# Performance work log

Measured on AMD Instinct MI355X. Metric: run time of the kernel, lower is better.

Reference implementation:

```python
import jax, jax.numpy as jnp
import numpy as np

N_NODES = 20000
N_EDGES = 320000
NUM_FEATURES = 128
HIDDEN = 128
NUM_CLASSES = 40
GRID_SIZE = 4
SPLINE_ORDER = 3
NB = GRID_SIZE + SPLINE_ORDER  # basis functions per input feature
_H = 2.0 / GRID_SIZE  # grid_range [-1, 1]
GRID = jnp.arange(-SPLINE_ORDER, GRID_SIZE + SPLINE_ORDER + 1, dtype=jnp.float32) * _H - 1.0


def b_splines(x):
    # x: (N, in) -> (N, in, NB) via Cox-de Boor recursion (efficient-KAN)
    xg = x[..., None]
    b = ((xg >= GRID[:-1]) & (xg < GRID[1:])).astype(x.dtype)
    for k in range(1, SPLINE_ORDER + 1):
        b = ((xg - GRID[: -(k + 1)]) / (GRID[k:-1] - GRID[: -(k + 1)]) * b[..., :-1]
             + (GRID[k + 1:] - xg) / (GRID[k + 1:] - GRID[1:-k]) * b[..., 1:])
    return b


def kan_linear(x, base_w, spline_w):
    # base branch: silu(x) @ W_base^T ; spline branch: contraction over (in, NB)
    base = jax.nn.silu(x) @ base_w.T
    spline = jnp.einsum('nik,oik->no', b_splines(x), spline_w)
    return base + spline


def gcn_conv(h, base_w, spline_w, bias, src_f, dst_f, norm):
    h = kan_linear(h, base_w, spline_w)
    msg = h[src_f] * norm[:, None]  # gather + edge scaling
    out = jax.ops.segment_sum(msg, dst_f, num_segments=N_NODES)
    return out + bias


def batchnorm(h, gamma, beta):
    mean = h.mean(axis=0)
    var = h.var(axis=0)  # biased, as torch BN uses for normalization
    return (h - mean) * jax.lax.rsqrt(var + 1e-5) * gamma + beta


def setup_inputs() -> dict:
    key = jax.random.key(0)
    ks = jax.random.split(key, 8)
    s = 0.1
    return {
        'x': jax.random.normal(ks[0], (N_NODES, NUM_FEATURES), dtype=jnp.float32),
        'edge_index': jax.random.randint(ks[1], (2, N_EDGES), 0, N_NODES, dtype=jnp.int64),
        'base_w0': jax.random.normal(ks[2], (HIDDEN, NUM_FEATURES), dtype=jnp.float32) * s,
        'spline_w0': jax.random.normal(ks[3], (HIDDEN, NUM_FEATURES, NB), dtype=jnp.float32) * s,
        'bias0': jnp.zeros((HIDDEN,), dtype=jnp.float32),
        'base_w1': jax.random.normal(ks[4], (HIDDEN, HIDDEN), dtype=jnp.float32) * s,
        'spline_w1': jax.random.normal(ks[5], (HIDDEN, HIDDEN, NB), dtype=jnp.float32) * s,
        'bias1': jnp.zeros((HIDDEN,), dtype=jnp.float32),
        'base_w_out': jax.random.normal(ks[6], (NUM_CLASSES, NUM_FEATURES + 2 * HIDDEN), dtype=jnp.float32) * s,
        'spline_w_out': jax.random.normal(ks[7], (NUM_CLASSES, NUM_FEATURES + 2 * HIDDEN, NB), dtype=jnp.float32) * s,
        'bias_out': jnp.zeros((NUM_CLASSES,), dtype=jnp.float32),
        'gamma': jnp.ones((HIDDEN,), dtype=jnp.float32),
        'beta': jnp.zeros((HIDDEN,), dtype=jnp.float32),
    }


def reference(x, edge_index, base_w0, spline_w0, bias0, base_w1, spline_w1, bias1,
              base_w_out, spline_w_out, bias_out, gamma, beta):
    # gcn_norm with self loops (computed once, reused by every layer)
    loop = jnp.arange(N_NODES, dtype=edge_index.dtype)
    src_f = jnp.concatenate([edge_index[0], loop])
    dst_f = jnp.concatenate([edge_index[1], loop])
    deg = jax.ops.segment_sum(jnp.ones_like(dst_f, dtype=x.dtype), dst_f, num_segments=N_NODES)
    dinv = jnp.where(deg > 0, jax.lax.rsqrt(jnp.maximum(deg, 1e-12)), 0.0)
    norm = dinv[src_f] * dinv[dst_f]

    skips = [x]
    h = x
    for bw, sw, b in ((base_w0, spline_w0, bias0), (base_w1, spline_w1, bias1)):
        h = gcn_conv(h, bw, sw, b, src_f, dst_f, norm)
        h = batchnorm(h, gamma, beta)  # shared BN, dropout p=0.0 is identity
        skips.append(h)
    h = jnp.concatenate(skips, axis=1)  # (N, 128 + 2*128)
    return gcn_conv(h, base_w_out, spline_w_out, bias_out, src_f, dst_f, norm)
```

## Files before the change

### kernel.cpp

```cpp
#include <hip/hip_runtime.h>

#define NN 20000
#define NPAD 20064

typedef _Float16 half8 __attribute__((ext_vector_type(8)));
typedef _Float16 half2v __attribute__((ext_vector_type(2)));
typedef float floatx4 __attribute__((ext_vector_type(4)));

#define MFMA16(a, b, c) __builtin_amdgcn_mfma_f32_16x16x32_f16((a), (b), (c), 0, 0, 0)
#define LD8(p) (*(const half8*)(p))
#define SBAR() __builtin_amdgcn_sched_barrier(0)

__device__ __forceinline__ void bspline7(float x, float b[7]) {
  float t[10];
#pragma unroll
  for (int i = 0; i < 10; ++i) {
    float g = -2.5f + 0.5f * (float)i;
    t[i] = (x >= g && x < g + 0.5f) ? 1.0f : 0.0f;
  }
#pragma unroll
  for (int i = 0; i < 9; ++i) {
    float g = -2.5f + 0.5f * (float)i;
    t[i] = ((x - g) * t[i] + (g + 1.0f - x) * t[i + 1]) * 2.0f;
  }
#pragma unroll
  for (int i = 0; i < 8; ++i) {
    float g = -2.5f + 0.5f * (float)i;
    t[i] = ((x - g) * t[i] + (g + 1.5f - x) * t[i + 1]);
  }
#pragma unroll
  for (int i = 0; i < 7; ++i) {
    float g = -2.5f + 0.5f * (float)i;
    b[i] = ((x - g) * t[i] + (g + 2.0f - x) * t[i + 1]) * (1.0f / 1.5f);
  }
}

__device__ __forceinline__ float silu_f(float x) {
  return x * (1.0f / (1.0f + __expf(-x)));
}

__device__ __forceinline__ void build_lds(const float* __restrict__ X,
                                          const float* __restrict__ ss, int has_bn,
                                          int row0, int tid, _Float16* __restrict__ Fs) {
  for (int idx = tid; idx < 32 * 128; idx += 256) {
    int r = idx >> 7, i = idx & 127;
    int row = row0 + r;
    float xv = (row < NN) ? X[(size_t)row * 128 + i] : 0.0f;
    if (has_bn) xv = xv * ss[i] + ss[128 + i];
    float b[7];
    bspline7(xv, b);
    half8 hv;
    hv[0] = (_Float16)silu_f(xv);
#pragma unroll
    for (int k = 0; k < 7; ++k) hv[k + 1] = (_Float16)b[k];
    *(half8*)(Fs + ((size_t)r * 128 + (i ^ (r & 7))) * 8) = hv;
  }
}

__global__ void packw_all(const float* __restrict__ Wb0, const float* __restrict__ Ws0,
                          const float* __restrict__ Wb1, const float* __restrict__ Ws1,
                          const float* __restrict__ WbO, const float* __restrict__ WsO,
                          _Float16* __restrict__ WPA0, _Float16* __restrict__ WPA1,
                          _Float16* __restrict__ WPC) {
  int bid = blockIdx.x;
  if (bid < 1536) {
    int s = (bid >= 768) ? 1 : 0;
    int idx = (bid - s * 768) * 256 + threadIdx.x;
    if (idx >= 196608) return;
    const float* Wb = s ? Wb1 : Wb0;
    const float* Wsp = s ? Ws1 : Ws0;
    _Float16* WP = s ? WPA1 : WPA0;
    int jj = idx & 7;
    int lane = (idx >> 3) & 63;
    int u = idx >> 9;
    int cb = u % 12, ks = u / 12;
    int i = ks * 4 + (lane >> 4);
    int orow = lane & 15;
    float v = 0.0f;
    if (cb < 8) {
      int o = cb * 16 + orow;
      v = (jj == 0) ? Wb[(size_t)o * 128 + i] : Wsp[(size_t)o * 896 + i * 7 + (jj - 1)];
    } else {
      int o = (cb - 8) * 16 + orow;
      if (o < 40)
        v = (jj == 0) ? WbO[(size_t)o * 384 + s * 128 + i]
                      : WsO[(size_t)o * 2688 + s * 896 + i * 7 + (jj - 1)];
    }
    WP[idx] = (_Float16)v;
  } else {
    int idx = (bid - 1536) * 256 + threadIdx.x;
    if (idx >= 65536) return;
    int jj = idx & 7;
    int lane = (idx >> 3) & 63;
    int u = idx >> 9;
    int cb = u & 3, ks = u >> 2;
    int i = ks * 4 + (lane >> 4);
    int o = cb * 16 + (lane & 15);
    float v = 0.0f;
    if (o < 40)
      v = (jj == 0) ? WbO[(size_t)o * 384 + 2 * 128 + i]
                    : WsO[(size_t)o * 2688 + 2 * 896 + i * 7 + (jj - 1)];
    WPC[idx] = (_Float16)v;
  }
}

__global__ void count_deg(const int* __restrict__ dst, int* __restrict__ degE, int E) {
  int e = blockIdx.x * 256 + threadIdx.x;
  if (e < E) atomicAdd(&degE[dst[e]], 1);
}

__global__ void build_meta2(const int* __restrict__ degE, int* __restrict__ rowptr,
                            int* __restrict__ cursor, float* __restrict__ dinv, int n) {
  __shared__ int wsum[16];
  int tid = threadIdx.x, lane = tid & 63, wid = tid >> 6;
  int i0 = tid * 20;
  int d[20];
  int s = 0;
#pragma unroll
  for (int j = 0; j < 20; ++j) {
    int i = i0 + j;
    int v = (i < n) ? degE[i] : 0;
    d[j] = v;
    s += v;
    if (i < n) dinv[i] = rsqrtf((float)(v + 1));
  }
  int val = s;
#pragma unroll
  for (int off = 1; off < 64; off <<= 1) {
    int t = __shfl_up(val, off);
    if (lane >= off) val += t;
  }
  if (lane == 63) wsum[wid] = val;
  __syncthreads();
  if (wid == 0) {
    int wv = (lane < 16) ? wsum[lane] : 0;
#pragma unroll
    for (int off = 1; off < 16; off <<= 1) {
      int t = __shfl_up(wv, off);
      if (lane >= off) wv += t;
    }
    if (lane < 16) wsum[lane] = wv;
  }
  __syncthreads();
  int base = (wid ? wsum[wid - 1] : 0) + val - s;
  if (tid == 0) rowptr[0] = 0;
#pragma unroll
  for (int j = 0; j < 20; ++j) {
    int i = i0 + j;
    if (i < n) {
      cursor[i] = base;
      rowptr[i + 1] = base + d[j];
      base += d[j];
    }
  }
}

__global__ void fill_csr(const int* __restrict__ src, const int* __restrict__ dst,
                         int* __restrict__ cursor, int* __restrict__ csr, int E) {
  int e = blockIdx.x * 256 + threadIdx.x;
  if (e < E) {
    int p = atomicAdd(&cursor[dst[e]], 1);
    csr[p] = src[e];
  }
}

__global__ __launch_bounds__(256) void gemmFA(const float* __restrict__ X,
                                              const float* __restrict__ ss, int has_bn,
                                              const _Float16* __restrict__ WP,
                                              const float* __restrict__ dinv,
                                              _Float16* __restrict__ A, float* __restrict__ P) {
  __shared__ _Float16 Fs[32 * 1024];
  int tid = threadIdx.x;
  int lane = tid & 63, cg = tid >> 6;
  int row0 = blockIdx.x * 32;
  build_lds(X, ss, has_bn, row0, tid, Fs);
  __syncthreads();
  int rx = lane & 7, kg = lane >> 4;
  const _Float16* Fr0 = Fs + (size_t)(lane & 15) * 1024;
  const _Float16* Fr1 = Fr0 + 16 * 1024;
  const _Float16* Bp = WP + ((size_t)(cg * 3) * 64 + lane) * 8;
  floatx4 acc0 = {}, acc1 = {}, acc2 = {}, acc3 = {}, acc4 = {}, acc5 = {};
  half8 xb0 = LD8(Bp), xb1 = LD8(Bp + 512), xb2 = LD8(Bp + 1024);
  half8 yb0 = LD8(Bp + 6144), yb1 = LD8(Bp + 6144 + 512), yb2 = LD8(Bp + 6144 + 1024);
#pragma unroll 1
  for (int ks = 0; ks < 32; ks += 2) {
    half8 a0 = LD8(Fr0 + (size_t)((ks * 4 + kg) ^ rx) * 8);
    half8 a1 = LD8(Fr1 + (size_t)((ks * 4 + kg) ^ rx) * 8);
    SBAR();
    acc0 = MFMA16(a0, xb0, acc0);
    acc1 = MFMA16(a0, xb1, acc1);
    acc2 = MFMA16(a0, xb2, acc2);
    acc3 = MFMA16(a1, xb0, acc3);
    acc4 = MFMA16(a1, xb1, acc4);
    acc5 = MFMA16(a1, xb2, acc5);
    SBAR();
    {
      const _Float16* bn = Bp + (size_t)(ks + 2) * 6144;
      xb0 = LD8(bn); xb1 = LD8(bn + 512); xb2 = LD8(bn + 1024);
    }
    half8 c0 = LD8(Fr0 + (size_t)(((ks + 1) * 4 + kg) ^ rx) * 8);
    half8 c1 = LD8(Fr1 + (size_t)(((ks + 1) * 4 + kg) ^ rx) * 8);
    SBAR();
    acc0 = MFMA16(c0, yb0, acc0);
    acc1 = MFMA16(c0, yb1, acc1);
    acc2 = MFMA16(c0, yb2, acc2);
    acc3 = MFMA16(c1, yb0, acc3);
    acc4 = MFMA16(c1, yb1, acc4);
    acc5 = MFMA16(c1, yb2, acc5);
    SBAR();
    {
      const _Float16* bn = Bp + (size_t)(ks + 3) * 6144;
      yb0 = LD8(bn); yb1 = LD8(bn + 512); yb2 = LD8(bn + 1024);
    }
    SBAR();
  }
  int oc = lane & 15;
  floatx4 accs[2][3] = {{acc0, acc1, acc2}, {acc3, acc4, acc5}};
#pragma unroll
  for (int rg = 0; rg < 2; ++rg) {
    int r0 = row0 + rg * 16 + (lane >> 4) * 4;
#pragma unroll
    for (int q = 0; q < 3; ++q) {
      int cb = cg * 3 + q;
      if (cb < 8) {
#pragma unroll
        for (int t = 0; t < 4; ++t)
          A[(size_t)(r0 + t) * 128 + cb * 16 + oc] = (_Float16)(accs[rg][q][t] * dinv[r0 + t]);
      } else {
#pragma unroll
        for (int t = 0; t < 4; ++t) P[(size_t)(r0 + t) * 64 + (cb - 8) * 16 + oc] = accs[rg][q][t];
      }
    }
  }
}

__global__ __launch_bounds__(256) void gemmFC(const float* __restrict__ X,
                                              const float* __restrict__ ss,
                                              const _Float16* __restrict__ WP,
                                              const float* __restrict__ P0,
                                              const float* __restrict__ P1,
                                              const float* __restrict__ dinv,
                                              _Float16* __restrict__ C) {
  __shared__ _Float16 Fs[32 * 1024];
  int tid = threadIdx.x;
  int lane = tid & 63, cg = tid >> 6;
  int row0 = blockIdx.x * 32;
  build_lds(X, ss, 1, row0, tid, Fs);
  __syncthreads();
  int rx = lane & 7, kg = lane >> 4;
  const _Float16* Fr0 = Fs + (size_t)(lane & 15) * 1024;
  const _Float16* Fr1 = Fr0 + 16 * 1024;
  const _Float16* Bp = WP + ((size_t)cg * 64 + lane) * 8;
  floatx4 acc0 = {}, acc1 = {};
  half8 xb = LD8(Bp), yb = LD8(Bp + 2048);
#pragma unroll 1
  for (int ks = 0; ks < 32; ks += 2) {
    half8 a0 = LD8(Fr0 + (size_t)((ks * 4 + kg) ^ rx) * 8);
    half8 a1 = LD8(Fr1 + (size_t)((ks * 4 + kg) ^ rx) * 8);
    SBAR();
    acc0 = MFMA16(a0, xb, acc0);
    acc1 = MFMA16(a1, xb, acc1);
    SBAR();
    xb = LD8(Bp + (size_t)(ks + 2) * 2048);
    half8 c0 = LD8(Fr0 + (size_t)(((ks + 1) * 4 + kg) ^ rx) * 8);
    half8 c1 = LD8(Fr1 + (size_t)(((ks + 1) * 4 + kg) ^ rx) * 8);
    SBAR();
    acc0 = MFMA16(c0, yb, acc0);
    acc1 = MFMA16(c1, yb, acc1);
    SBAR();
    yb = LD8(Bp + (size_t)(ks + 3) * 2048);
    SBAR();
  }
  int oc = lane & 15;
  floatx4 accs[2] = {acc0, acc1};
#pragma unroll
  for (int rg = 0; rg < 2; ++rg) {
    int r0 = row0 + rg * 16 + (lane >> 4) * 4;
#pragma unroll
    for (int t = 0; t < 4; ++t) {
      size_t idx = (size_t)(r0 + t) * 64 + cg * 16 + oc;
      C[idx] = (_Float16)((accs[rg][t] + P0[idx] + P1[idx]) * dinv[r0 + t]);
    }
  }
}

__global__ __launch_bounds__(256) void aggregate128h(const _Float16* __restrict__ Ah,
                                                     const int* __restrict__ rowptr,
                                                     const int* __restrict__ csr,
                                                     const float* __restrict__ dinv,
                                                     const float* __restrict__ bias,
                                                     float* __restrict__ Y) {
  int wid = threadIdx.x >> 6, lane = threadIdx.x & 63;
  int n = blockIdx.x * 4 + wid;
  float di = dinv[n];
  half2v self = *(const half2v*)(Ah + (size_t)n * 128 + lane * 2);
  float a0 = (float)self[0], a1 = (float)self[1];
  float b0x = 0, b0y = 0, b1x = 0, b1y = 0, b2x = 0, b2y = 0, b3x = 0, b3y = 0;
  int e0 = rowptr[n], m = rowptr[n + 1] - e0;
  int j = 0;
  for (; j + 4 <= m; j += 4) {
    int s0 = csr[e0 + j], s1 = csr[e0 + j + 1], s2 = csr[e0 + j + 2], s3 = csr[e0 + j + 3];
    half2v r0 = *(const half2v*)(Ah + (size_t)s0 * 128 + lane * 2);
    half2v r1 = *(const half2v*)(Ah + (size_t)s1 * 128 + lane * 2);
    half2v r2 = *(const half2v*)(Ah + (size_t)s2 * 128 + lane * 2);
    half2v r3 = *(const half2v*)(Ah + (size_t)s3 * 128 + lane * 2);
    b0x += (float)r0[0]; b0y += (float)r0[1];
    b1x += (float)r1[0]; b1y += (float)r1[1];
    b2x += (float)r2[0]; b2y += (float)r2[1];
    b3x += (float)r3[0]; b3y += (float)r3[1];
  }
  for (; j < m; ++j) {
    int s = csr[e0 + j];
    half2v r = *(const half2v*)(Ah + (size_t)s * 128 + lane * 2);
    b0x += (float)r[0]; b0y += (float)r[1];
  }
  a0 += (b0x + b1x) + (b2x + b3x);
  a1 += (b0y + b1y) + (b2y + b3y);
  float2 outv = {a0 * di + bias[lane * 2], a1 * di + bias[lane * 2 + 1]};
  *(float2*)(Y + (size_t)n * 128 + lane * 2) = outv;
}

__global__ __launch_bounds__(256) void aggregate40h(const _Float16* __restrict__ Ch,
                                                    const int* __restrict__ rowptr,
                                                    const int* __restrict__ csr,
                                                    const float* __restrict__ dinv,
                                                    const float* __restrict__ bias,
                                                    float* __restrict__ out) {
  int wid = threadIdx.x >> 6, lane = threadIdx.x & 63;
  int n = blockIdx.x * 4 + wid;
  float di = dinv[n];
  float a = (float)Ch[(size_t)n * 64 + lane];
  float b0 = 0, b1 = 0, b2 = 0, b3 = 0;
  int e0 = rowptr[n], m = rowptr[n + 1] - e0;
  int j = 0;
  for (; j + 4 <= m; j += 4) {
    int s0 = csr[e0 + j], s1 = csr[e0 + j + 1], s2 = csr[e0 + j + 2], s3 = csr[e0 + j + 3];
    b0 += (float)Ch[(size_t)s0 * 64 + lane];
    b1 += (float)Ch[(size_t)s1 * 64 + lane];
    b2 += (float)Ch[(size_t)s2 * 64 + lane];
    b3 += (float)Ch[(size_t)s3 * 64 + lane];
  }
  for (; j < m; ++j) {
    int s = csr[e0 + j];
    b0 += (float)Ch[(size_t)s * 64 + lane];
  }
  a += (b0 + b1) + (b2 + b3);
  if (lane < 40) out[(size_t)n * 40 + lane] = a * di + bias[lane];
}

__global__ __launch_bounds__(256) void bn_stats(const float* __restrict__ H,
                                                float* __restrict__ partial) {
  int tid = threadIdx.x;
  int c4 = (tid & 31) * 4;
  int r0 = blockIdx.x * 32 + (tid >> 5) * 4;
  float s0 = 0, s1 = 0, s2 = 0, s3 = 0, q0 = 0, q1 = 0, q2 = 0, q3 = 0;
#pragma unroll
  for (int j = 0; j < 4; ++j) {
    float4 v = *(const float4*)(H + (size_t)(r0 + j) * 128 + c4);
    s0 += v.x; s1 += v.y; s2 += v.z; s3 += v.w;
    q0 += v.x * v.x; q1 += v.y * v.y; q2 += v.z * v.z; q3 += v.w * v.w;
  }
  __shared__ float sh[2][256][4];
  sh[0][tid][0] = s0; sh[0][tid][1] = s1; sh[0][tid][2] = s2; sh[0][tid][3] = s3;
  sh[1][tid][0] = q0; sh[1][tid][1] = q1; sh[1][tid][2] = q2; sh[1][tid][3] = q3;
  __syncthreads();
  if (tid < 32) {
    float a0 = 0, a1 = 0, a2 = 0, a3 = 0, b0 = 0, b1 = 0, b2 = 0, b3 = 0;
#pragma unroll
    for (int g = 0; g < 8; ++g) {
      int u = g * 32 + tid;
      a0 += sh[0][u][0]; a1 += sh[0][u][1]; a2 += sh[0][u][2]; a3 += sh[0][u][3];
      b0 += sh[1][u][0]; b1 += sh[1][u][1]; b2 += sh[1][u][2]; b3 += sh[1][u][3];
    }
    float* p = partial + (size_t)blockIdx.x * 256;
    p[tid * 4 + 0] = a0; p[tid * 4 + 1] = a1; p[tid * 4 + 2] = a2; p[tid * 4 + 3] = a3;
    p[128 + tid * 4 + 0] = b0; p[128 + tid * 4 + 1] = b1;
    p[128 + tid * 4 + 2] = b2; p[128 + tid * 4 + 3] = b3;
  }
}

__global__ __launch_bounds__(256) void bn_reduce(const float* __restrict__ partial,
                                                 float* __restrict__ p2) {
  int tid = threadIdx.x;
  const float* base = partial + (size_t)blockIdx.x * 25 * 256 + tid;
  float a0 = 0, a1 = 0, a2 = 0, a3 = 0, a4 = 0;
#pragma unroll
  for (int j = 0; j < 5; ++j) {
    a0 += base[(j * 5 + 0) * 256];
    a1 += base[(j * 5 + 1) * 256];
    a2 += base[(j * 5 + 2) * 256];
    a3 += base[(j * 5 + 3) * 256];
    a4 += base[(j * 5 + 4) * 256];
  }
  p2[(size_t)blockIdx.x * 256 + tid] = ((a0 + a1) + (a2 + a3)) + a4;
}

__global__ __launch_bounds__(256) void bn_final2(const float* __restrict__ p2,
                                                 const float* __restrict__ gamma,
                                                 const float* __restrict__ beta,
                                                 float* __restrict__ ss) {
  int tid = threadIdx.x;
  double a0 = 0, a1 = 0, a2 = 0, a3 = 0, a4 = 0;
#pragma unroll
  for (int j = 0; j < 5; ++j) {
    a0 += (double)p2[(size_t)(j * 5 + 0) * 256 + tid];
    a1 += (double)p2[(size_t)(j * 5 + 1) * 256 + tid];
    a2 += (double)p2[(size_t)(j * 5 + 2) * 256 + tid];
    a3 += (double)p2[(size_t)(j * 5 + 3) * 256 + tid];
    a4 += (double)p2[(size_t)(j * 5 + 4) * 256 + tid];
  }
  double tot = ((a0 + a1) + (a2 + a3)) + a4;
  __shared__ double sh[256];
  sh[tid] = tot;
  __syncthreads();
  if (tid < 128) {
    double S = sh[tid];
    double Q = sh[128 + tid];
    double mean = S / (double)NN;
    double var = Q / (double)NN - mean * mean;
    float sc = gamma[tid] * rsqrtf((float)var + 1e-5f);
    ss[tid] = sc;
    ss[128 + tid] = beta[tid] - (float)mean * sc;
  }
}

extern "C" void kernel_launch(void* const* d_in, const int* in_sizes, int n_in,
                              void* d_out, int out_size, void* d_ws, size_t ws_size,
                              hipStream_t stream) {
  const float* x = (const float*)d_in[0];
  const int* ei = (const int*)d_in[1];
  const float* bw0 = (const float*)d_in[2];
  const float* sw0 = (const float*)d_in[3];
  const float* b0 = (const float*)d_in[4];
  const float* bw1 = (const float*)d_in[5];
  const float* sw1 = (const float*)d_in[6];
  const float* b1 = (const float*)d_in[7];
  const float* bwo = (const float*)d_in[8];
  const float* swo = (const float*)d_in[9];
  const float* bo = (const float*)d_in[10];
  const float* gamma = (const float*)d_in[11];
  const float* beta = (const float*)d_in[12];
  const int E = in_sizes[1] / 2;
  const int* esrc = ei;
  const int* edst = ei + E;

  char* ws = (char*)d_ws;
  size_t off = 0;
  auto alloc = [&](size_t bytes) -> void* {
    void* p = ws + off;
    off = (off + bytes + 255) & ~(size_t)255;
    return p;
  };
  _Float16* WPA0 = (_Float16*)alloc((196608 + 16384) * 2);
  _Float16* WPA1 = (_Float16*)alloc((196608 + 16384) * 2);
  _Float16* WPC = (_Float16*)alloc((65536 + 16384) * 2);
  float* dinv = (float*)alloc(NPAD * 4);
  int* degE = (int*)alloc(NN * 4);
  int* rowptr = (int*)alloc((NN + 1) * 4);
  int* cursor = (int*)alloc(NN * 4);
  int* csr = (int*)alloc((size_t)E * 4);
  _Float16* A = (_Float16*)alloc((size_t)NPAD * 128 * 2);
  float* h1 = (float*)alloc((size_t)NN * 128 * 4);
  float* P0 = (float*)alloc((size_t)NPAD * 64 * 4);
  float* P1 = (float*)alloc((size_t)NPAD * 64 * 4);
  _Float16* Ch = (_Float16*)alloc((size_t)NPAD * 64 * 2);
  float* partial = (float*)alloc((size_t)625 * 256 * 4);
  float* p2 = (float*)alloc((size_t)25 * 256 * 4);
  float* ssb = (float*)alloc(256 * 4);
  float* h2 = h1;
  (void)ws_size; (void)n_in; (void)out_size;

  int egrid = (E + 255) / 256;
  const int GG = 626;

  hipMemsetAsync(degE, 0, NN * sizeof(int), stream);
  packw_all<<<1792, 256, 0, stream>>>(bw0, sw0, bw1, sw1, bwo, swo, WPA0, WPA1, WPC);
  count_deg<<<egrid, 256, 0, stream>>>(edst, degE, E);
  build_meta2<<<1, 1024, 0, stream>>>(degE, rowptr, cursor, dinv, NN);
  fill_csr<<<egrid, 256, 0, stream>>>(esrc, edst, cursor, csr, E);

  gemmFA<<<GG, 256, 0, stream>>>(x, ssb, 0, WPA0, dinv, A, P0);
  aggregate128h<<<5000, 256, 0, stream>>>(A, rowptr, csr, dinv, b0, h1);
  bn_stats<<<625, 256, 0, stream>>>(h1, partial);
  bn_reduce<<<25, 256, 0, stream>>>(partial, p2);
  bn_final2<<<1, 256, 0, stream>>>(p2, gamma, beta, ssb);

  gemmFA<<<GG, 256, 0, stream>>>(h1, ssb, 1, WPA1, dinv, A, P1);
  aggregate128h<<<5000, 256, 0, stream>>>(A, rowptr, csr, dinv, b1, h2);
  bn_stats<<<625, 256, 0, stream>>>(h2, partial);
  bn_reduce<<<25, 256, 0, stream>>>(partial, p2);
  bn_final2<<<1, 256, 0, stream>>>(p2, gamma, beta, ssb);

  gemmFC<<<GG, 256, 0, stream>>>(h2, ssb, WPC, P0, P1, dinv, Ch);
  aggregate40h<<<5000, 256, 0, stream>>>(Ch, rowptr, csr, dinv, bo, (float*)d_out);
}
```

Measured before the change: 250.0 us.

## Use 16-row GEMM tiles and closed-form cubic B-spline basis

```diff
diff --git a/kernel.cpp b/kernel.cpp
--- a/kernel.cpp
+++ b/kernel.cpp
@@ -1,7 +1,6 @@
 #include <hip/hip_runtime.h>
 
 #define NN 20000
-#define NPAD 20064
 
 typedef _Float16 half8 __attribute__((ext_vector_type(8)));
 typedef _Float16 half2v __attribute__((ext_vector_type(2)));
@@ -11,27 +10,23 @@
 #define LD8(p) (*(const half8*)(p))
 #define SBAR() __builtin_amdgcn_sched_barrier(0)
 
-__device__ __forceinline__ void bspline7(float x, float b[7]) {
-  float t[10];
-#pragma unroll
-  for (int i = 0; i < 10; ++i) {
-    float g = -2.5f + 0.5f * (float)i;
-    t[i] = (x >= g && x < g + 0.5f) ? 1.0f : 0.0f;
-  }
-#pragma unroll
-  for (int i = 0; i < 9; ++i) {
-    float g = -2.5f + 0.5f * (float)i;
-    t[i] = ((x - g) * t[i] + (g + 1.0f - x) * t[i + 1]) * 2.0f;
-  }
-#pragma unroll
-  for (int i = 0; i < 8; ++i) {
-    float g = -2.5f + 0.5f * (float)i;
-    t[i] = ((x - g) * t[i] + (g + 1.5f - x) * t[i + 1]);
-  }
+__device__ __forceinline__ void bspline7_fast(float x, float b[7]) {
+  float u = (x + 2.5f) * 2.0f;
+  float cf = floorf(u);
+  int c = (int)cf;
+  float t = u - cf;
+  float omt = 1.0f - t;
+  float t2 = t * t, t3 = t2 * t;
+  float w0 = omt * omt * omt * (1.0f / 6.0f);
+  float w1 = (3.0f * t3 - 6.0f * t2 + 4.0f) * (1.0f / 6.0f);
+  float w2 = (-3.0f * t3 + 3.0f * t2 + 3.0f * t + 1.0f) * (1.0f / 6.0f);
+  float w3 = t3 * (1.0f / 6.0f);
+  bool valid = (c >= 0) && (c <= 9);
 #pragma unroll
   for (int i = 0; i < 7; ++i) {
-    float g = -2.5f + 0.5f * (float)i;
-    b[i] = ((x - g) * t[i] + (g + 2.0f - x) * t[i + 1]) * (1.0f / 1.5f);
+    int d = c - i;
+    float w = (d == 0) ? w3 : (d == 1) ? w2 : (d == 2) ? w1 : (d == 3) ? w0 : 0.0f;
+    b[i] = valid ? w : 0.0f;
   }
 }
 
@@ -39,16 +34,17 @@
   return x * (1.0f / (1.0f + __expf(-x)));
 }
 
-__device__ __forceinline__ void build_lds(const float* __restrict__ X,
-                                          const float* __restrict__ ss, int has_bn,
-                                          int row0, int tid, _Float16* __restrict__ Fs) {
-  for (int idx = tid; idx < 32 * 128; idx += 256) {
+__device__ __forceinline__ void build_lds16(const float* __restrict__ X,
+                                            const float* __restrict__ ss, int has_bn,
+                                            int row0, int tid, _Float16* __restrict__ Fs) {
+#pragma unroll
+  for (int it = 0; it < 8; ++it) {
+    int idx = it * 256 + tid;
     int r = idx >> 7, i = idx & 127;
-    int row = row0 + r;
-    float xv = (row < NN) ? X[(size_t)row * 128 + i] : 0.0f;
+    float xv = X[(size_t)(row0 + r) * 128 + i];
     if (has_bn) xv = xv * ss[i] + ss[128 + i];
     float b[7];
-    bspline7(xv, b);
+    bspline7_fast(xv, b);
     half8 hv;
     hv[0] = (_Float16)silu_f(xv);
 #pragma unroll
@@ -169,44 +165,35 @@
                                               const _Float16* __restrict__ WP,
                                               const float* __restrict__ dinv,
                                               _Float16* __restrict__ A, float* __restrict__ P) {
-  __shared__ _Float16 Fs[32 * 1024];
+  __shared__ _Float16 Fs[16 * 1024];
   int tid = threadIdx.x;
   int lane = tid & 63, cg = tid >> 6;
-  int row0 = blockIdx.x * 32;
-  build_lds(X, ss, has_bn, row0, tid, Fs);
+  int row0 = blockIdx.x * 16;
+  build_lds16(X, ss, has_bn, row0, tid, Fs);
   __syncthreads();
   int rx = lane & 7, kg = lane >> 4;
-  const _Float16* Fr0 = Fs + (size_t)(lane & 15) * 1024;
-  const _Float16* Fr1 = Fr0 + 16 * 1024;
+  const _Float16* Fr = Fs + (size_t)(lane & 15) * 1024;
   const _Float16* Bp = WP + ((size_t)(cg * 3) * 64 + lane) * 8;
-  floatx4 acc0 = {}, acc1 = {}, acc2 = {}, acc3 = {}, acc4 = {}, acc5 = {};
+  floatx4 acc0 = {}, acc1 = {}, acc2 = {};
   half8 xb0 = LD8(Bp), xb1 = LD8(Bp + 512), xb2 = LD8(Bp + 1024);
   half8 yb0 = LD8(Bp + 6144), yb1 = LD8(Bp + 6144 + 512), yb2 = LD8(Bp + 6144 + 1024);
 #pragma unroll 1
   for (int ks = 0; ks < 32; ks += 2) {
-    half8 a0 = LD8(Fr0 + (size_t)((ks * 4 + kg) ^ rx) * 8);
-    half8 a1 = LD8(Fr1 + (size_t)((ks * 4 + kg) ^ rx) * 8);
+    half8 a0 = LD8(Fr + (size_t)((ks * 4 + kg) ^ rx) * 8);
     SBAR();
     acc0 = MFMA16(a0, xb0, acc0);
     acc1 = MFMA16(a0, xb1, acc1);
     acc2 = MFMA16(a0, xb2, acc2);
-    acc3 = MFMA16(a1, xb0, acc3);
-    acc4 = MFMA16(a1, xb1, acc4);
-    acc5 = MFMA16(a1, xb2, acc5);
     SBAR();
     {
       const _Float16* bn = Bp + (size_t)(ks + 2) * 6144;
       xb0 = LD8(bn); xb1 = LD8(bn + 512); xb2 = LD8(bn + 1024);
     }
-    half8 c0 = LD8(Fr0 + (size_t)(((ks + 1) * 4 + kg) ^ rx) * 8);
-    half8 c1 = LD8(Fr1 + (size_t)(((ks + 1) * 4 + kg) ^ rx) * 8);
+    half8 c0 = LD8(Fr + (size_t)(((ks + 1) * 4 + kg) ^ rx) * 8);
     SBAR();
     acc0 = MFMA16(c0, yb0, acc0);
     acc1 = MFMA16(c0, yb1, acc1);
     acc2 = MFMA16(c0, yb2, acc2);
-    acc3 = MFMA16(c1, yb0, acc3);
-    acc4 = MFMA16(c1, yb1, acc4);
-    acc5 = MFMA16(c1, yb2, acc5);
     SBAR();
     {
       const _Float16* bn = Bp + (size_t)(ks + 3) * 6144;
@@ -215,21 +202,18 @@
     SBAR();
   }
   int oc = lane & 15;
-  floatx4 accs[2][3] = {{acc0, acc1, acc2}, {acc3, acc4, acc5}};
-#pragma unroll
-  for (int rg = 0; rg < 2; ++rg) {
-    int r0 = row0 + rg * 16 + (lane >> 4) * 4;
-#pragma unroll
-    for (int q = 0; q < 3; ++q) {
-      int cb = cg * 3 + q;
-      if (cb < 8) {
-#pragma unroll
-        for (int t = 0; t < 4; ++t)
-          A[(size_t)(r0 + t) * 128 + cb * 16 + oc] = (_Float16)(accs[rg][q][t] * dinv[r0 + t]);
-      } else {
-#pragma unroll
-        for (int t = 0; t < 4; ++t) P[(size_t)(r0 + t) * 64 + (cb - 8) * 16 + oc] = accs[rg][q][t];
-      }
+  int r0 = row0 + (lane >> 4) * 4;
+  floatx4 accs[3] = {acc0, acc1, acc2};
+#pragma unroll
+  for (int q = 0; q < 3; ++q) {
+    int cb = cg * 3 + q;
+    if (cb < 8) {
+#pragma unroll
+      for (int t = 0; t < 4; ++t)
+        A[(size_t)(r0 + t) * 128 + cb * 16 + oc] = (_Float16)(accs[q][t] * dinv[r0 + t]);
+    } else {
+#pragma unroll
+      for (int t = 0; t < 4; ++t) P[(size_t)(r0 + t) * 64 + (cb - 8) * 16 + oc] = accs[q][t];
     }
   }
 }
@@ -241,46 +225,37 @@
                                               const float* __restrict__ P1,
                                               const float* __restrict__ dinv,
                                               _Float16* __restrict__ C) {
-  __shared__ _Float16 Fs[32 * 1024];
+  __shared__ _Float16 Fs[16 * 1024];
   int tid = threadIdx.x;
   int lane = tid & 63, cg = tid >> 6;
-  int row0 = blockIdx.x * 32;
-  build_lds(X, ss, 1, row0, tid, Fs);
+  int row0 = blockIdx.x * 16;
+  build_lds16(X, ss, 1, row0, tid, Fs);
   __syncthreads();
   int rx = lane & 7, kg = lane >> 4;
-  const _Float16* Fr0 = Fs + (size_t)(lane & 15) * 1024;
-  const _Float16* Fr1 = Fr0 + 16 * 1024;
+  const _Float16* Fr = Fs + (size_t)(lane & 15) * 1024;
   const _Float16* Bp = WP + ((size_t)cg * 64 + lane) * 8;
-  floatx4 acc0 = {}, acc1 = {};
+  floatx4 acc0 = {};
   half8 xb = LD8(Bp), yb = LD8(Bp + 2048);
 #pragma unroll 1
   for (int ks = 0; ks < 32; ks += 2) {
-    half8 a0 = LD8(Fr0 + (size_t)((ks * 4 + kg) ^ rx) * 8);
-    half8 a1 = LD8(Fr1 + (size_t)((ks * 4 + kg) ^ rx) * 8);
+    half8 a0 = LD8(Fr + (size_t)((ks * 4 + kg) ^ rx) * 8);
     SBAR();
     acc0 = MFMA16(a0, xb, acc0);
-    acc1 = MFMA16(a1, xb, acc1);
     SBAR();
     xb = LD8(Bp + (size_t)(ks + 2) * 2048);
-    half8 c0 = LD8(Fr0 + (size_t)(((ks + 1) * 4 + kg) ^ rx) * 8);
-    half8 c1 = LD8(Fr1 + (size_t)(((ks + 1) * 4 + kg) ^ rx) * 8);
+    half8 c0 = LD8(Fr + (size_t)(((ks + 1) * 4 + kg) ^ rx) * 8);
     SBAR();
     acc0 = MFMA16(c0, yb, acc0);
-    acc1 = MFMA16(c1, yb, acc1);
     SBAR();
     yb = LD8(Bp + (size_t)(ks + 3) * 2048);
     SBAR();
   }
   int oc = lane & 15;
-  floatx4 accs[2] = {acc0, acc1};
-#pragma unroll
-  for (int rg = 0; rg < 2; ++rg) {
-    int r0 = row0 + rg * 16 + (lane >> 4) * 4;
-#pragma unroll
-    for (int t = 0; t < 4; ++t) {
-      size_t idx = (size_t)(r0 + t) * 64 + cg * 16 + oc;
-      C[idx] = (_Float16)((accs[rg][t] + P0[idx] + P1[idx]) * dinv[r0 + t]);
-    }
+  int r0 = row0 + (lane >> 4) * 4;
+#pragma unroll
+  for (int t = 0; t < 4; ++t) {
+    size_t idx = (size_t)(r0 + t) * 64 + cg * 16 + oc;
+    C[idx] = (_Float16)((acc0[t] + P0[idx] + P1[idx]) * dinv[r0 + t]);
   }
 }
 
@@ -454,16 +429,16 @@
   _Float16* WPA0 = (_Float16*)alloc((196608 + 16384) * 2);
   _Float16* WPA1 = (_Float16*)alloc((196608 + 16384) * 2);
   _Float16* WPC = (_Float16*)alloc((65536 + 16384) * 2);
-  float* dinv = (float*)alloc(NPAD * 4);
+  float* dinv = (float*)alloc(NN * 4);
   int* degE = (int*)alloc(NN * 4);
   int* rowptr = (int*)alloc((NN + 1) * 4);
   int* cursor = (int*)alloc(NN * 4);
   int* csr = (int*)alloc((size_t)E * 4);
-  _Float16* A = (_Float16*)alloc((size_t)NPAD * 128 * 2);
+  _Float16* A = (_Float16*)alloc((size_t)NN * 128 * 2);
   float* h1 = (float*)alloc((size_t)NN * 128 * 4);
-  float* P0 = (float*)alloc((size_t)NPAD * 64 * 4);
-  float* P1 = (float*)alloc((size_t)NPAD * 64 * 4);
-  _Float16* Ch = (_Float16*)alloc((size_t)NPAD * 64 * 2);
+  float* P0 = (float*)alloc((size_t)NN * 64 * 4);
+  float* P1 = (float*)alloc((size_t)NN * 64 * 4);
+  _Float16* Ch = (_Float16*)alloc((size_t)NN * 64 * 2);
   float* partial = (float*)alloc((size_t)625 * 256 * 4);
   float* p2 = (float*)alloc((size_t)25 * 256 * 4);
   float* ssb = (float*)alloc(256 * 4);
@@ -471,7 +446,7 @@
   (void)ws_size; (void)n_in; (void)out_size;
 
   int egrid = (E + 255) / 256;
-  const int GG = 626;
+  const int GG = 1250;
 
   hipMemsetAsync(degE, 0, NN * sizeof(int), stream);
   packw_all<<<1792, 256, 0, stream>>>(bw0, sw0, bw1, sw1, bwo, swo, WPA0, WPA1, WPC);
```

Result: no change. 248.0 us (-0.8%).
